# Kernel optimization log

Measured on AMD Instinct MI355X. Metric: run time of the kernel, lower is better.

The kernel has to match this reference:

```python
import jax, jax.numpy as jnp
import numpy as np

N, E = 50000, 800000
IN_CH, HID, OUT, EDIM = 151, 128, 51, 51


def setup_inputs() -> dict:
    key = jax.random.key(0)
    ks = jax.random.split(key, 10)
    def w(k, shape, fan_in):
        return jax.random.normal(k, shape, jnp.float32) * (1.0 / np.sqrt(fan_in))
    return {
        "x": jax.random.normal(ks[0], (N, IN_CH), jnp.float32),
        "edge_attr": jax.random.normal(ks[1], (E, EDIM), jnp.float32),
        "W_edge0": w(ks[2], (EDIM, IN_CH), EDIM),
        "b_edge0": jnp.zeros((IN_CH,), jnp.float32),
        "W0": w(ks[3], (IN_CH, HID), IN_CH),
        "b0": jnp.zeros((HID,), jnp.float32),
        "W_edge1": w(ks[4], (EDIM, HID), EDIM),
        "b_edge1": jnp.zeros((HID,), jnp.float32),
        "W1": w(ks[5], (HID, HID), HID),
        "b1": jnp.zeros((HID,), jnp.float32),
        "W_out": w(ks[6], (HID, OUT), HID),
        "b_out": jnp.zeros((OUT,), jnp.float32),
        "edge_index": jax.random.randint(ks[7], (2, E), 0, N, jnp.int32),
    }


def gtn_layer(x, src, dst, edge_attr, W_e, b_e, W, b):
    # message: x_j + Linear(edge_attr);  aggr='add' scatter to dst.
    eat = edge_attr @ W_e + b_e                                # [E, in_ch]
    msgs = x[src] + eat                                        # gather + add
    agg = jax.ops.segment_sum(msgs, dst, num_segments=x.shape[0])
    # self-loops carry zero edge_attr -> transformed attr == bias b_e,
    # so their message is x + b_e (equivalent to concatenating N self-loop edges).
    agg = agg + x + b_e
    return agg @ W + b                                         # self.linear


def reference(x, edge_attr, W_edge0, b_edge0, W0, b0, W_edge1, b_edge1, W1, b1, W_out, b_out, edge_index):
    src, dst = edge_index[0], edge_index[1]
    h = gtn_layer(x, src, dst, edge_attr, W_edge0, b_edge0, W0, b0)   # [N, HID]
    h = gtn_layer(h, src, dst, edge_attr, W_edge1, b_edge1, W1, b1)   # [N, HID]
    # global_mean_pool with batch=arange(N) is identity (one node per graph)
    return h @ W_out + b_out                                          # [N, OUT]
```

## Files before the change

kernel.cpp:

```cpp
#include <hip/hip_runtime.h>

#define N_NODES 50000
#define N_EDGES 800000
#define IN_CH   151
#define HID     128
#define OUT_CH  51
#define EDIM    51
#define SSTR    52
#define WP      64
#define LSTR    68
#define NBLK    ((N_NODES + 255) / 256)
#define EBLK    ((N_EDGES + 255) / 256)
#define KW1_T   (51 * 128 + 128 + 128 * WP)
#define KW1_B   ((KW1_T + 255) / 256)
#define KW2_T   (51 * WP + 102)
#define KW2_B   ((KW2_T + 255) / 256)

static __device__ __forceinline__ unsigned int f2bf(float f) {
    union { float f; unsigned int u; } v; v.f = f;
    unsigned int r = v.u + 0x7FFF + ((v.u >> 16) & 1);
    return r >> 16;
}
static __device__ __forceinline__ float bflo(unsigned int u) {
    return __uint_as_float(u << 16);
}
static __device__ __forceinline__ float bfhi(unsigned int u) {
    return __uint_as_float(u & 0xFFFF0000u);
}

__global__ void k_hist_kw1(const int* __restrict__ ei, int* __restrict__ deg,
                           const float* __restrict__ We0, const float* __restrict__ W0,
                           const float* __restrict__ be0, const float* __restrict__ W1,
                           const float* __restrict__ Wout,
                           float* __restrict__ M0, float* __restrict__ c0,
                           float* __restrict__ Wc) {
    if (blockIdx.x < EBLK) {
        int e = blockIdx.x * 256 + threadIdx.x;
        if (e < N_EDGES) atomicAdd(&deg[ei[N_EDGES + e]], 1);
        return;
    }
    int t = (blockIdx.x - EBLK) * 256 + threadIdx.x;
    if (t < 51 * 128) {
        int i = t / 128, j = t % 128;
        float a = 0.f;
        for (int k = 0; k < IN_CH; ++k) a += We0[i * IN_CH + k] * W0[k * HID + j];
        M0[t] = a;
    } else if (t < 51 * 128 + 128) {
        int j = t - 51 * 128;
        float a = 0.f;
        for (int k = 0; k < IN_CH; ++k) a += be0[k] * W0[k * HID + j];
        c0[j] = a;
    } else if (t < 51 * 128 + 128 + 128 * WP) {
        int u = t - (51 * 128 + 128);
        int i = u / WP, j = u % WP;
        float a = 0.f;
        if (j < OUT_CH)
            for (int k = 0; k < HID; ++k) a += W1[i * HID + k] * Wout[k * OUT_CH + j];
        Wc[i * WP + j] = a;
    }
}

__global__ void k_scan1_kw2(const int* __restrict__ deg, int* __restrict__ blksum,
                            const float* __restrict__ We1, const float* __restrict__ be1,
                            const float* __restrict__ b1, const float* __restrict__ Wout,
                            const float* __restrict__ bout, const float* __restrict__ Wc,
                            float* __restrict__ Mc, float* __restrict__ cc,
                            float* __restrict__ dd) {
    if (blockIdx.x < NBLK) {
        __shared__ int lds[256];
        int i = blockIdx.x * 256 + threadIdx.x;
        lds[threadIdx.x] = (i < N_NODES) ? deg[i] : 0;
        __syncthreads();
        for (int s = 128; s > 0; s >>= 1) {
            if (threadIdx.x < s) lds[threadIdx.x] += lds[threadIdx.x + s];
            __syncthreads();
        }
        if (threadIdx.x == 0) blksum[blockIdx.x] = lds[0];
        return;
    }
    int t = (blockIdx.x - NBLK) * 256 + threadIdx.x;
    if (t < 51 * WP) {
        int i = t / WP, j = t % WP;
        float a = 0.f;
        if (j < OUT_CH)
            for (int k = 0; k < HID; ++k) a += We1[i * HID + k] * Wc[k * WP + j];
        Mc[t] = a;
    } else if (t < 51 * WP + 51) {
        int j = t - 51 * WP;
        float a = 0.f;
        for (int k = 0; k < HID; ++k) a += be1[k] * Wc[k * WP + j];
        cc[j] = a;
    } else if (t < 51 * WP + 102) {
        int j = t - (51 * WP + 51);
        float a = 0.f;
        for (int k = 0; k < HID; ++k) a += b1[k] * Wout[k * OUT_CH + j];
        dd[j] = a + bout[j];
    }
}

__global__ void k_scan3m(const int* __restrict__ deg, const int* __restrict__ blksum,
                         int* __restrict__ row_start, int* __restrict__ cursor) {
    __shared__ int lds[256];
    __shared__ int s_off;
    int tid = threadIdx.x;
    int v2 = (tid < NBLK) ? blksum[tid] : 0;
    lds[tid] = v2;
    __syncthreads();
    for (int s = 1; s < 256; s <<= 1) {
        int t = (tid >= s) ? lds[tid - s] : 0;
        __syncthreads();
        lds[tid] += t;
        __syncthreads();
    }
    if (tid == 0) s_off = (blockIdx.x == 0) ? 0 : lds[blockIdx.x - 1];
    __syncthreads();
    int boff = s_off;
    int i = blockIdx.x * 256 + tid;
    int v = (i < N_NODES) ? deg[i] : 0;
    lds[tid] = v;
    __syncthreads();
    for (int s = 1; s < 256; s <<= 1) {
        int t = (tid >= s) ? lds[tid - s] : 0;
        __syncthreads();
        lds[tid] += t;
        __syncthreads();
    }
    if (i < N_NODES) {
        int ex = boff + lds[tid] - v;
        row_start[i] = ex;
        cursor[i] = ex;
    }
    if (blockIdx.x == 0 && tid == 0) row_start[N_NODES] = N_EDGES;
}

__global__ void k_fill(const int* __restrict__ ei, int* __restrict__ cursor,
                       int2* __restrict__ pairs) {
    int e = blockIdx.x * 256 + threadIdx.x;
    if (e >= N_EDGES) return;
    int src = ei[e];
    int dst = ei[N_EDGES + e];
    int pos = atomicAdd(&cursor[dst], 1);
    pairs[pos] = make_int2(src, e);
}

__global__ void k_agg_S(const float* __restrict__ ea, const int2* __restrict__ pairs,
                        const int* __restrict__ row_start, float* __restrict__ S) {
    int n = blockIdx.x * 4 + (threadIdx.x >> 6);
    if (n >= N_NODES) return;
    int lane = threadIdx.x & 63;
    int g = lane >> 4, sub = lane & 15;
    int n0 = row_start[n], n1 = row_start[n + 1];
    float4 acc = make_float4(0.f, 0.f, 0.f, 0.f);
    for (int base = n0; base < n1; base += 64) {
        int cnt = min(64, n1 - base);
        int eid_l = (base + lane < n1) ? pairs[base + lane].y : 0;
        for (int t = 0; t < cnt; t += 4) {
            int idx = t + g;
            bool ok = idx < cnt;
            int e = __shfl(eid_l, ok ? idx : 0);
            if (ok && sub < 13) {
                float4 v = *(const float4*)(ea + (size_t)e * EDIM + sub * 4);
                if (sub == 12) v.w = 0.f;
                acc.x += v.x; acc.y += v.y; acc.z += v.z; acc.w += v.w;
            }
        }
    }
    acc.x += __shfl_xor(acc.x, 16); acc.y += __shfl_xor(acc.y, 16);
    acc.z += __shfl_xor(acc.z, 16); acc.w += __shfl_xor(acc.w, 16);
    acc.x += __shfl_xor(acc.x, 32); acc.y += __shfl_xor(acc.y, 32);
    acc.z += __shfl_xor(acc.z, 32); acc.w += __shfl_xor(acc.w, 32);
    if (lane < 13)
        *(float4*)(S + (size_t)n * SSTR + lane * 4) = acc;
}

__global__ void k_agg_h(const uint4* __restrict__ yb4, const int2* __restrict__ pairs,
                        const int* __restrict__ row_start, float* __restrict__ hacc) {
    int n = blockIdx.x * 4 + (threadIdx.x >> 6);
    if (n >= N_NODES) return;
    int lane = threadIdx.x & 63;
    int g = lane >> 4, s = lane & 15;
    int n0 = row_start[n], n1 = row_start[n + 1];
    float acc[8];
#pragma unroll
    for (int j = 0; j < 8; ++j) acc[j] = 0.f;
    for (int base = n0; base < n1; base += 64) {
        int cnt = min(64, n1 - base);
        int s_l = (base + lane < n1) ? pairs[base + lane].x : 0;
        for (int t = 0; t < cnt; t += 4) {
            int idx = t + g;
            bool ok = idx < cnt;
            int srcn = __shfl(s_l, ok ? idx : 0);
            if (ok) {
                uint4 v = yb4[(size_t)srcn * 16 + s];
                acc[0] += bflo(v.x); acc[1] += bfhi(v.x);
                acc[2] += bflo(v.y); acc[3] += bfhi(v.y);
                acc[4] += bflo(v.z); acc[5] += bfhi(v.z);
                acc[6] += bflo(v.w); acc[7] += bfhi(v.w);
            }
        }
    }
#pragma unroll
    for (int j = 0; j < 8; ++j) {
        acc[j] += __shfl_xor(acc[j], 16);
        acc[j] += __shfl_xor(acc[j], 32);
    }
    if (lane < 16) {
        float4* hp = (float4*)(hacc + (size_t)n * HID + lane * 8);
        float4 a = hp[0], b = hp[1];
        a.x += acc[0]; a.y += acc[1]; a.z += acc[2]; a.w += acc[3];
        b.x += acc[4]; b.y += acc[5]; b.z += acc[6]; b.w += acc[7];
        hp[0] = a; hp[1] = b;
    }
}

__global__ void k_agg_out(const uint4* __restrict__ wb4, const int2* __restrict__ pairs,
                          const int* __restrict__ row_start, float* __restrict__ out) {
    int n = blockIdx.x * 4 + (threadIdx.x >> 6);
    if (n >= N_NODES) return;
    int lane = threadIdx.x & 63;
    int g = lane >> 3, s = lane & 7;
    int n0 = row_start[n], n1 = row_start[n + 1];
    float acc[8];
#pragma unroll
    for (int j = 0; j < 8; ++j) acc[j] = 0.f;
    for (int base = n0; base < n1; base += 64) {
        int cnt = min(64, n1 - base);
        int s_l = (base + lane < n1) ? pairs[base + lane].x : 0;
        for (int t = 0; t < cnt; t += 8) {
            int idx = t + g;
            bool ok = idx < cnt;
            int srcn = __shfl(s_l, ok ? idx : 0);
            if (ok) {
                uint4 v = wb4[(size_t)srcn * 8 + s];
                acc[0] += bflo(v.x); acc[1] += bfhi(v.x);
                acc[2] += bflo(v.y); acc[3] += bfhi(v.y);
                acc[4] += bflo(v.z); acc[5] += bfhi(v.z);
                acc[6] += bflo(v.w); acc[7] += bfhi(v.w);
            }
        }
    }
#pragma unroll
    for (int j = 0; j < 8; ++j) {
        acc[j] += __shfl_xor(acc[j], 8);
        acc[j] += __shfl_xor(acc[j], 16);
        acc[j] += __shfl_xor(acc[j], 32);
    }
    if (lane < 8) {
#pragma unroll
        for (int j = 0; j < 8; ++j) {
            int ch = lane * 8 + j;
            if (ch < OUT_CH) out[(size_t)n * OUT_CH + ch] += acc[j];
        }
    }
}

__global__ __launch_bounds__(256, 4) void k_layer0(
        const float* __restrict__ x, const float* __restrict__ W0,
        const float* __restrict__ b0, const float* __restrict__ S,
        const int* __restrict__ deg, const float* __restrict__ M0,
        const float* __restrict__ c0,
        unsigned int* __restrict__ yb, float* __restrict__ hacc) {
    __shared__ float aT[64 * LSTR];
    int tid = threadIdx.x;
    int r_base = blockIdx.x * 64;
    int cg = tid & 15, rg = tid >> 4;
    int c = cg * 8, r0 = rg * 4;

    float4 accA[4], accB[4];
#pragma unroll
    for (int i = 0; i < 4; ++i) {
        accA[i] = make_float4(0.f, 0.f, 0.f, 0.f);
        accB[i] = make_float4(0.f, 0.f, 0.f, 0.f);
    }

    for (int p = 0; p < 3; ++p) {
        int koff = p * 64;
        int chunk = min(64, IN_CH - koff);
        __syncthreads();
        for (int idx = tid; idx < 64 * 64; idx += 256) {
            int r = idx >> 6, kk = idx & 63;
            if (kk >= chunk) continue;
            int row = r_base + r;
            aT[kk * LSTR + r] = (row < N_NODES) ? x[(size_t)row * IN_CH + koff + kk] : 0.f;
        }
        __syncthreads();
#pragma unroll 4
        for (int kk = 0; kk < chunk; ++kk) {
            int k = koff + kk;
            float4 wv0 = *(const float4*)(W0 + k * HID + c);
            float4 wv1 = *(const float4*)(W0 + k * HID + c + 4);
            float4 a0 = *(const float4*)(&aT[kk * LSTR + r0]);
            float ar[4] = {a0.x, a0.y, a0.z, a0.w};
#pragma unroll
            for (int i = 0; i < 4; ++i) {
                accA[i].x += ar[i] * wv0.x; accA[i].y += ar[i] * wv0.y;
                accA[i].z += ar[i] * wv0.z; accA[i].w += ar[i] * wv0.w;
                accB[i].x += ar[i] * wv1.x; accB[i].y += ar[i] * wv1.y;
                accB[i].z += ar[i] * wv1.z; accB[i].w += ar[i] * wv1.w;
            }
        }
    }

#pragma unroll
    for (int i = 0; i < 4; ++i) {
        int row = r_base + r0 + i;
        if (row < N_NODES) {
            uint4 pk;
            pk.x = f2bf(accA[i].x) | (f2bf(accA[i].y) << 16);
            pk.y = f2bf(accA[i].z) | (f2bf(accA[i].w) << 16);
            pk.z = f2bf(accB[i].x) | (f2bf(accB[i].y) << 16);
            pk.w = f2bf(accB[i].z) | (f2bf(accB[i].w) << 16);
            *(uint4*)(yb + (size_t)row * 64 + (c >> 1)) = pk;
        }
    }

    __syncthreads();
    for (int idx = tid; idx < 64 * 64; idx += 256) {
        int r = idx >> 6, kk = idx & 63;
        if (kk >= EDIM) continue;
        int row = r_base + r;
        aT[kk * LSTR + r] = (row < N_NODES) ? S[(size_t)row * SSTR + kk] : 0.f;
    }
    __syncthreads();
#pragma unroll 4
    for (int kk = 0; kk < EDIM; ++kk) {
        float4 wv0 = *(const float4*)(M0 + kk * HID + c);
        float4 wv1 = *(const float4*)(M0 + kk * HID + c + 4);
        float4 a0 = *(const float4*)(&aT[kk * LSTR + r0]);
        float ar[4] = {a0.x, a0.y, a0.z, a0.w};
#pragma unroll
        for (int i = 0; i < 4; ++i) {
            accA[i].x += ar[i] * wv0.x; accA[i].y += ar[i] * wv0.y;
            accA[i].z += ar[i] * wv0.z; accA[i].w += ar[i] * wv0.w;
            accB[i].x += ar[i] * wv1.x; accB[i].y += ar[i] * wv1.y;
            accB[i].z += ar[i] * wv1.z; accB[i].w += ar[i] * wv1.w;
        }
    }

    float4 cv0 = *(const float4*)(c0 + c);
    float4 cv1 = *(const float4*)(c0 + c + 4);
    float4 bv0 = *(const float4*)(b0 + c);
    float4 bv1 = *(const float4*)(b0 + c + 4);
#pragma unroll
    for (int i = 0; i < 4; ++i) {
        int row = r_base + r0 + i;
        if (row < N_NODES) {
            float d1 = (float)(deg[row] + 1);
            float4 vA = accA[i], vB = accB[i];
            vA.x += d1 * cv0.x + bv0.x; vA.y += d1 * cv0.y + bv0.y;
            vA.z += d1 * cv0.z + bv0.z; vA.w += d1 * cv0.w + bv0.w;
            vB.x += d1 * cv1.x + bv1.x; vB.y += d1 * cv1.y + bv1.y;
            vB.z += d1 * cv1.z + bv1.z; vB.w += d1 * cv1.w + bv1.w;
            *(float4*)(hacc + (size_t)row * HID + c) = vA;
            *(float4*)(hacc + (size_t)row * HID + c + 4) = vB;
        }
    }
}

__global__ __launch_bounds__(256, 4) void k_layer1(
        const float* __restrict__ hacc, const float* __restrict__ Wc,
        const float* __restrict__ S, const int* __restrict__ deg,
        const float* __restrict__ Mc, const float* __restrict__ cc,
        const float* __restrict__ dd,
        unsigned int* __restrict__ wb, float* __restrict__ out) {
    __shared__ float aT[64 * LSTR];
    int tid = threadIdx.x;
    int r_base = blockIdx.x * 64;
    int cg = tid & 15, rg = tid >> 4;
    int c = cg * 4, r0 = rg * 4;

    float4 acc[4];
#pragma unroll
    for (int i = 0; i < 4; ++i) acc[i] = make_float4(0.f, 0.f, 0.f, 0.f);

    for (int p = 0; p < 2; ++p) {
        int koff = p * 64;
        __syncthreads();
        for (int idx = tid; idx < 64 * 64; idx += 256) {
            int r = idx >> 6, kk = idx & 63;
            int row = r_base + r;
            aT[kk * LSTR + r] = (row < N_NODES) ? hacc[(size_t)row * HID + koff + kk] : 0.f;
        }
        __syncthreads();
#pragma unroll 4
        for (int kk = 0; kk < 64; ++kk) {
            int k = koff + kk;
            float4 wv = *(const float4*)(Wc + k * WP + c);
            float4 a0 = *(const float4*)(&aT[kk * LSTR + r0]);
            float ar[4] = {a0.x, a0.y, a0.z, a0.w};
#pragma unroll
            for (int i = 0; i < 4; ++i) {
                acc[i].x += ar[i] * wv.x; acc[i].y += ar[i] * wv.y;
                acc[i].z += ar[i] * wv.z; acc[i].w += ar[i] * wv.w;
            }
        }
    }

#pragma unroll
    for (int i = 0; i < 4; ++i) {
        int row = r_base + r0 + i;
        if (row < N_NODES) {
            uint2 pk;
            pk.x = f2bf(acc[i].x) | (f2bf(acc[i].y) << 16);
            pk.y = f2bf(acc[i].z) | (f2bf(acc[i].w) << 16);
            *(uint2*)(wb + (size_t)row * 32 + (c >> 1)) = pk;
        }
    }

    __syncthreads();
    for (int idx = tid; idx < 64 * 64; idx += 256) {
        int r = idx >> 6, kk = idx & 63;
        if (kk >= EDIM) continue;
        int row = r_base + r;
        aT[kk * LSTR + r] = (row < N_NODES) ? S[(size_t)row * SSTR + kk] : 0.f;
    }
    __syncthreads();
#pragma unroll 4
    for (int kk = 0; kk < EDIM; ++kk) {
        float4 wv = *(const float4*)(Mc + kk * WP + c);
        float4 a0 = *(const float4*)(&aT[kk * LSTR + r0]);
        float ar[4] = {a0.x, a0.y, a0.z, a0.w};
#pragma unroll
        for (int i = 0; i < 4; ++i) {
            acc[i].x += ar[i] * wv.x; acc[i].y += ar[i] * wv.y;
            acc[i].z += ar[i] * wv.z; acc[i].w += ar[i] * wv.w;
        }
    }

    if (c < OUT_CH) {
        float cv[4], dv[4];
#pragma unroll
        for (int j = 0; j < 4; ++j) {
            int col = c + j;
            cv[j] = (col < OUT_CH) ? cc[col] : 0.f;
            dv[j] = (col < OUT_CH) ? dd[col] : 0.f;
        }
#pragma unroll
        for (int i = 0; i < 4; ++i) {
            int row = r_base + r0 + i;
            if (row < N_NODES) {
                float d1 = (float)(deg[row] + 1);
                const float* ap = (const float*)&acc[i];
#pragma unroll
                for (int j = 0; j < 4; ++j) {
                    int col = c + j;
                    if (col < OUT_CH)
                        out[(size_t)row * OUT_CH + col] = ap[j] + d1 * cv[j] + dv[j];
                }
            }
        }
    }
}

extern "C" void kernel_launch(void* const* d_in, const int* in_sizes, int n_in,
                              void* d_out, int out_size, void* d_ws, size_t ws_size,
                              hipStream_t stream) {
    const float* x    = (const float*)d_in[0];
    const float* ea   = (const float*)d_in[1];
    const float* We0  = (const float*)d_in[2];
    const float* be0  = (const float*)d_in[3];
    const float* W0   = (const float*)d_in[4];
    const float* b0   = (const float*)d_in[5];
    const float* We1  = (const float*)d_in[6];
    const float* be1  = (const float*)d_in[7];
    const float* W1   = (const float*)d_in[8];
    const float* b1   = (const float*)d_in[9];
    const float* Wout = (const float*)d_in[10];
    const float* bout = (const float*)d_in[11];
    const int*   ei   = (const int*)d_in[12];
    float* out = (float*)d_out;

    char* p = (char*)d_ws;
    auto alloc = [&](size_t bytes) {
        char* r = p;
        p += (bytes + 255) & ~(size_t)255;
        return r;
    };
    float* S         = (float*)alloc((size_t)N_NODES * SSTR * 4);
    int*   deg       = (int*)  alloc((size_t)N_NODES * 4);
    int*   row_start = (int*)  alloc((size_t)(N_NODES + 1) * 4);
    int*   cursor    = (int*)  alloc((size_t)N_NODES * 4);
    int*   blksum    = (int*)  alloc((size_t)NBLK * 4);
    int2*  pairs     = (int2*) alloc((size_t)N_EDGES * 8);
    unsigned int* yb = (unsigned int*)alloc((size_t)N_NODES * 64 * 4);
    float* hacc      = (float*)alloc((size_t)N_NODES * HID * 4);
    unsigned int* wb = (unsigned int*)alloc((size_t)N_NODES * 32 * 4);
    float* M0        = (float*)alloc(51 * 128 * 4);
    float* c0        = (float*)alloc(128 * 4);
    float* Wc        = (float*)alloc(128 * WP * 4);
    float* Mc        = (float*)alloc(51 * WP * 4);
    float* cc        = (float*)alloc(51 * 4);
    float* dd        = (float*)alloc(51 * 4);

    hipMemsetAsync(deg, 0, (size_t)N_NODES * 4, stream);

    k_hist_kw1<<<EBLK + KW1_B, 256, 0, stream>>>(ei, deg, We0, W0, be0, W1, Wout, M0, c0, Wc);
    k_scan1_kw2<<<NBLK + KW2_B, 256, 0, stream>>>(deg, blksum, We1, be1, b1, Wout, bout,
                                                  Wc, Mc, cc, dd);
    k_scan3m<<<NBLK, 256, 0, stream>>>(deg, blksum, row_start, cursor);
    k_fill<<<EBLK, 256, 0, stream>>>(ei, cursor, pairs);

    k_agg_S<<<(N_NODES + 3) / 4, 256, 0, stream>>>(ea, pairs, row_start, S);

    k_layer0<<<(N_NODES + 63) / 64, 256, 0, stream>>>(x, W0, b0, S, deg, M0, c0, yb, hacc);
    k_agg_h<<<(N_NODES + 3) / 4, 256, 0, stream>>>((const uint4*)yb, pairs, row_start, hacc);

    k_layer1<<<(N_NODES + 63) / 64, 256, 0, stream>>>(hacc, Wc, S, deg, Mc, cc, dd, wb, out);
    k_agg_out<<<(N_NODES + 3) / 4, 256, 0, stream>>>((const uint4*)wb, pairs, row_start, out);
}
```

Before: 587.2 us.

## Fuse edge-attr and neighbor aggregation into layer GEMM kernels

Moves the per-node edge_attr sum (S) into the start of the layer-0 GEMM kernel and the bf16 neighbor-feature gather into the start of the layer-1 GEMM kernel. Each block first aggregates its own 64 nodes, then reuses the result. Layer 1 keeps the gathered sums in a 32KB shared tile, which avoids a read-modify-write of hacc in global memory and removes two launches. In exchange, parallelism for the irregular gather drops from 4 nodes per block to 16 nodes per wave, which can hurt latency hiding. The extra shared memory also lowers occupancy, so launch bounds change to 3.

```diff
diff --git a/kernel.cpp b/kernel.cpp
--- a/kernel.cpp
+++ b/kernel.cpp
@@ -143,76 +143,6 @@
     pairs[pos] = make_int2(src, e);
 }
 
-__global__ void k_agg_S(const float* __restrict__ ea, const int2* __restrict__ pairs,
-                        const int* __restrict__ row_start, float* __restrict__ S) {
-    int n = blockIdx.x * 4 + (threadIdx.x >> 6);
-    if (n >= N_NODES) return;
-    int lane = threadIdx.x & 63;
-    int g = lane >> 4, sub = lane & 15;
-    int n0 = row_start[n], n1 = row_start[n + 1];
-    float4 acc = make_float4(0.f, 0.f, 0.f, 0.f);
-    for (int base = n0; base < n1; base += 64) {
-        int cnt = min(64, n1 - base);
-        int eid_l = (base + lane < n1) ? pairs[base + lane].y : 0;
-        for (int t = 0; t < cnt; t += 4) {
-            int idx = t + g;
-            bool ok = idx < cnt;
-            int e = __shfl(eid_l, ok ? idx : 0);
-            if (ok && sub < 13) {
-                float4 v = *(const float4*)(ea + (size_t)e * EDIM + sub * 4);
-                if (sub == 12) v.w = 0.f;
-                acc.x += v.x; acc.y += v.y; acc.z += v.z; acc.w += v.w;
-            }
-        }
-    }
-    acc.x += __shfl_xor(acc.x, 16); acc.y += __shfl_xor(acc.y, 16);
-    acc.z += __shfl_xor(acc.z, 16); acc.w += __shfl_xor(acc.w, 16);
-    acc.x += __shfl_xor(acc.x, 32); acc.y += __shfl_xor(acc.y, 32);
-    acc.z += __shfl_xor(acc.z, 32); acc.w += __shfl_xor(acc.w, 32);
-    if (lane < 13)
-        *(float4*)(S + (size_t)n * SSTR + lane * 4) = acc;
-}
-
-__global__ void k_agg_h(const uint4* __restrict__ yb4, const int2* __restrict__ pairs,
-                        const int* __restrict__ row_start, float* __restrict__ hacc) {
-    int n = blockIdx.x * 4 + (threadIdx.x >> 6);
-    if (n >= N_NODES) return;
-    int lane = threadIdx.x & 63;
-    int g = lane >> 4, s = lane & 15;
-    int n0 = row_start[n], n1 = row_start[n + 1];
-    float acc[8];
-#pragma unroll
-    for (int j = 0; j < 8; ++j) acc[j] = 0.f;
-    for (int base = n0; base < n1; base += 64) {
-        int cnt = min(64, n1 - base);
-        int s_l = (base + lane < n1) ? pairs[base + lane].x : 0;
-        for (int t = 0; t < cnt; t += 4) {
-            int idx = t + g;
-            bool ok = idx < cnt;
-            int srcn = __shfl(s_l, ok ? idx : 0);
-            if (ok) {
-                uint4 v = yb4[(size_t)srcn * 16 + s];
-                acc[0] += bflo(v.x); acc[1] += bfhi(v.x);
-                acc[2] += bflo(v.y); acc[3] += bfhi(v.y);
-                acc[4] += bflo(v.z); acc[5] += bfhi(v.z);
-                acc[6] += bflo(v.w); acc[7] += bfhi(v.w);
-            }
-        }
-    }
-#pragma unroll
-    for (int j = 0; j < 8; ++j) {
-        acc[j] += __shfl_xor(acc[j], 16);
-        acc[j] += __shfl_xor(acc[j], 32);
-    }
-    if (lane < 16) {
-        float4* hp = (float4*)(hacc + (size_t)n * HID + lane * 8);
-        float4 a = hp[0], b = hp[1];
-        a.x += acc[0]; a.y += acc[1]; a.z += acc[2]; a.w += acc[3];
-        b.x += acc[4]; b.y += acc[5]; b.z += acc[6]; b.w += acc[7];
-        hp[0] = a; hp[1] = b;
-    }
-}
-
 __global__ void k_agg_out(const uint4* __restrict__ wb4, const int2* __restrict__ pairs,
                           const int* __restrict__ row_start, float* __restrict__ out) {
     int n = blockIdx.x * 4 + (threadIdx.x >> 6);
@@ -254,15 +184,50 @@
     }
 }
 
-__global__ __launch_bounds__(256, 4) void k_layer0(
+__global__ __launch_bounds__(256, 4) void k_layer0f(
         const float* __restrict__ x, const float* __restrict__ W0,
-        const float* __restrict__ b0, const float* __restrict__ S,
+        const float* __restrict__ b0, const float* __restrict__ ea,
+        const int2* __restrict__ pairs, const int* __restrict__ row_start,
         const int* __restrict__ deg, const float* __restrict__ M0,
-        const float* __restrict__ c0,
+        const float* __restrict__ c0, float* __restrict__ S,
         unsigned int* __restrict__ yb, float* __restrict__ hacc) {
     __shared__ float aT[64 * LSTR];
     int tid = threadIdx.x;
     int r_base = blockIdx.x * 64;
+
+    {
+        int wv = tid >> 6;
+        int lane = tid & 63;
+        int g = lane >> 4, sub = lane & 15;
+        for (int u = 0; u < 16; ++u) {
+            int n = r_base + wv * 16 + u;
+            if (n >= N_NODES) break;
+            int n0 = row_start[n], n1 = row_start[n + 1];
+            float4 acc = make_float4(0.f, 0.f, 0.f, 0.f);
+            for (int base = n0; base < n1; base += 64) {
+                int cnt = min(64, n1 - base);
+                int eid_l = (base + lane < n1) ? pairs[base + lane].y : 0;
+                for (int t = 0; t < cnt; t += 4) {
+                    int idx = t + g;
+                    bool ok = idx < cnt;
+                    int e = __shfl(eid_l, ok ? idx : 0);
+                    if (ok && sub < 13) {
+                        float4 v = *(const float4*)(ea + (size_t)e * EDIM + sub * 4);
+                        if (sub == 12) v.w = 0.f;
+                        acc.x += v.x; acc.y += v.y; acc.z += v.z; acc.w += v.w;
+                    }
+                }
+            }
+            acc.x += __shfl_xor(acc.x, 16); acc.y += __shfl_xor(acc.y, 16);
+            acc.z += __shfl_xor(acc.z, 16); acc.w += __shfl_xor(acc.w, 16);
+            acc.x += __shfl_xor(acc.x, 32); acc.y += __shfl_xor(acc.y, 32);
+            acc.z += __shfl_xor(acc.z, 32); acc.w += __shfl_xor(acc.w, 32);
+            if (lane < 13)
+                *(float4*)(S + (size_t)n * SSTR + lane * 4) = acc;
+        }
+    }
+    __syncthreads();
+
     int cg = tid & 15, rg = tid >> 4;
     int c = cg * 8, r0 = rg * 4;
 
@@ -357,15 +322,59 @@
     }
 }
 
-__global__ __launch_bounds__(256, 4) void k_layer1(
+__global__ __launch_bounds__(256, 3) void k_layer1f(
         const float* __restrict__ hacc, const float* __restrict__ Wc,
         const float* __restrict__ S, const int* __restrict__ deg,
         const float* __restrict__ Mc, const float* __restrict__ cc,
-        const float* __restrict__ dd,
+        const float* __restrict__ dd, const uint4* __restrict__ yb4,
+        const int2* __restrict__ pairs, const int* __restrict__ row_start,
         unsigned int* __restrict__ wb, float* __restrict__ out) {
     __shared__ float aT[64 * LSTR];
+    __shared__ float gt[64 * 128];
     int tid = threadIdx.x;
     int r_base = blockIdx.x * 64;
+
+    {
+        int wv = tid >> 6;
+        int lane = tid & 63;
+        int g = lane >> 4, s = lane & 15;
+        for (int u = 0; u < 16; ++u) {
+            int n = r_base + wv * 16 + u;
+            if (n >= N_NODES) break;
+            int n0 = row_start[n], n1 = row_start[n + 1];
+            float acc[8];
+#pragma unroll
+            for (int j = 0; j < 8; ++j) acc[j] = 0.f;
+            for (int base = n0; base < n1; base += 64) {
+                int cnt = min(64, n1 - base);
+                int s_l = (base + lane < n1) ? pairs[base + lane].x : 0;
+                for (int t = 0; t < cnt; t += 4) {
+                    int idx = t + g;
+                    bool ok = idx < cnt;
+                    int srcn = __shfl(s_l, ok ? idx : 0);
+                    if (ok) {
+                        uint4 v = yb4[(size_t)srcn * 16 + s];
+                        acc[0] += bflo(v.x); acc[1] += bfhi(v.x);
+                        acc[2] += bflo(v.y); acc[3] += bfhi(v.y);
+                        acc[4] += bflo(v.z); acc[5] += bfhi(v.z);
+                        acc[6] += bflo(v.w); acc[7] += bfhi(v.w);
+                    }
+                }
+            }
+#pragma unroll
+            for (int j = 0; j < 8; ++j) {
+                acc[j] += __shfl_xor(acc[j], 16);
+                acc[j] += __shfl_xor(acc[j], 32);
+            }
+            if (lane < 16) {
+                float* gp = gt + (wv * 16 + u) * 128 + lane * 8;
+                *(float4*)(gp)     = make_float4(acc[0], acc[1], acc[2], acc[3]);
+                *(float4*)(gp + 4) = make_float4(acc[4], acc[5], acc[6], acc[7]);
+            }
+        }
+    }
+    __syncthreads();
+
     int cg = tid & 15, rg = tid >> 4;
     int c = cg * 4, r0 = rg * 4;
 
@@ -379,7 +388,9 @@
         for (int idx = tid; idx < 64 * 64; idx += 256) {
             int r = idx >> 6, kk = idx & 63;
             int row = r_base + r;
-            aT[kk * LSTR + r] = (row < N_NODES) ? hacc[(size_t)row * HID + koff + kk] : 0.f;
+            aT[kk * LSTR + r] = (row < N_NODES)
+                ? hacc[(size_t)row * HID + koff + kk] + gt[r * 128 + koff + kk]
+                : 0.f;
         }
         __syncthreads();
 #pragma unroll 4
@@ -500,11 +511,11 @@
     k_scan3m<<<NBLK, 256, 0, stream>>>(deg, blksum, row_start, cursor);
     k_fill<<<EBLK, 256, 0, stream>>>(ei, cursor, pairs);
 
-    k_agg_S<<<(N_NODES + 3) / 4, 256, 0, stream>>>(ea, pairs, row_start, S);
-
-    k_layer0<<<(N_NODES + 63) / 64, 256, 0, stream>>>(x, W0, b0, S, deg, M0, c0, yb, hacc);
-    k_agg_h<<<(N_NODES + 3) / 4, 256, 0, stream>>>((const uint4*)yb, pairs, row_start, hacc);
-
-    k_layer1<<<(N_NODES + 63) / 64, 256, 0, stream>>>(hacc, Wc, S, deg, Mc, cc, dd, wb, out);
+    k_layer0f<<<(N_NODES + 63) / 64, 256, 0, stream>>>(
+        x, W0, b0, ea, pairs, row_start, deg, M0, c0, S, yb, hacc);
+
+    k_layer1f<<<(N_NODES + 63) / 64, 256, 0, stream>>>(
+        hacc, Wc, S, deg, Mc, cc, dd, (const uint4*)yb, pairs, row_start, wb, out);
+
     k_agg_out<<<(N_NODES + 3) / 4, 256, 0, stream>>>((const uint4*)wb, pairs, row_start, out);
 }
```

Measured after the change: 670.6 us. 14.2% more time.

## Replace CSR gather of edge attrs with atomic scatter-add and shrink edge list

Applied to the files above, without the earlier changes.

The per-destination CSR gather of edge_attr rows into S is replaced by a grid-stride kernel that streams edge_attr linearly and atomically adds each element into S at its destination row. The CSR edge list now stores only source ids instead of (src, edge id) pairs, halving that buffer's traffic in fill and the two aggregation kernels. S is zeroed together with deg in one memset. The change trades random 204-byte row gathers for coalesced reads plus about 40M float atomics, which can contend and makes the S sums order-nondeterministic.

```diff
diff --git a/kernel.cpp b/kernel.cpp
--- a/kernel.cpp
+++ b/kernel.cpp
@@ -134,46 +134,29 @@
 }
 
 __global__ void k_fill(const int* __restrict__ ei, int* __restrict__ cursor,
-                       int2* __restrict__ pairs) {
+                       int* __restrict__ srcs) {
     int e = blockIdx.x * 256 + threadIdx.x;
     if (e >= N_EDGES) return;
     int src = ei[e];
     int dst = ei[N_EDGES + e];
     int pos = atomicAdd(&cursor[dst], 1);
-    pairs[pos] = make_int2(src, e);
-}
-
-__global__ void k_agg_S(const float* __restrict__ ea, const int2* __restrict__ pairs,
-                        const int* __restrict__ row_start, float* __restrict__ S) {
-    int n = blockIdx.x * 4 + (threadIdx.x >> 6);
-    if (n >= N_NODES) return;
-    int lane = threadIdx.x & 63;
-    int g = lane >> 4, sub = lane & 15;
-    int n0 = row_start[n], n1 = row_start[n + 1];
-    float4 acc = make_float4(0.f, 0.f, 0.f, 0.f);
-    for (int base = n0; base < n1; base += 64) {
-        int cnt = min(64, n1 - base);
-        int eid_l = (base + lane < n1) ? pairs[base + lane].y : 0;
-        for (int t = 0; t < cnt; t += 4) {
-            int idx = t + g;
-            bool ok = idx < cnt;
-            int e = __shfl(eid_l, ok ? idx : 0);
-            if (ok && sub < 13) {
-                float4 v = *(const float4*)(ea + (size_t)e * EDIM + sub * 4);
-                if (sub == 12) v.w = 0.f;
-                acc.x += v.x; acc.y += v.y; acc.z += v.z; acc.w += v.w;
-            }
-        }
-    }
-    acc.x += __shfl_xor(acc.x, 16); acc.y += __shfl_xor(acc.y, 16);
-    acc.z += __shfl_xor(acc.z, 16); acc.w += __shfl_xor(acc.w, 16);
-    acc.x += __shfl_xor(acc.x, 32); acc.y += __shfl_xor(acc.y, 32);
-    acc.z += __shfl_xor(acc.z, 32); acc.w += __shfl_xor(acc.w, 32);
-    if (lane < 13)
-        *(float4*)(S + (size_t)n * SSTR + lane * 4) = acc;
-}
-
-__global__ void k_agg_h(const uint4* __restrict__ yb4, const int2* __restrict__ pairs,
+    srcs[pos] = src;
+}
+
+__global__ void k_scatter_S(const float* __restrict__ ea, const int* __restrict__ ei,
+                            float* __restrict__ S) {
+    const unsigned int TOT = (unsigned int)N_EDGES * EDIM;
+    unsigned int stride = gridDim.x * blockDim.x;
+    for (unsigned int i = blockIdx.x * blockDim.x + threadIdx.x; i < TOT; i += stride) {
+        unsigned int e = i / EDIM;
+        unsigned int c = i - e * EDIM;
+        float v = ea[i];
+        int dst = ei[N_EDGES + e];
+        atomicAdd(&S[(size_t)dst * SSTR + c], v);
+    }
+}
+
+__global__ void k_agg_h(const uint4* __restrict__ yb4, const int* __restrict__ srcs,
                         const int* __restrict__ row_start, float* __restrict__ hacc) {
     int n = blockIdx.x * 4 + (threadIdx.x >> 6);
     if (n >= N_NODES) return;
@@ -185,7 +168,7 @@
     for (int j = 0; j < 8; ++j) acc[j] = 0.f;
     for (int base = n0; base < n1; base += 64) {
         int cnt = min(64, n1 - base);
-        int s_l = (base + lane < n1) ? pairs[base + lane].x : 0;
+        int s_l = (base + lane < n1) ? srcs[base + lane] : 0;
         for (int t = 0; t < cnt; t += 4) {
             int idx = t + g;
             bool ok = idx < cnt;
@@ -213,7 +196,7 @@
     }
 }
 
-__global__ void k_agg_out(const uint4* __restrict__ wb4, const int2* __restrict__ pairs,
+__global__ void k_agg_out(const uint4* __restrict__ wb4, const int* __restrict__ srcs,
                           const int* __restrict__ row_start, float* __restrict__ out) {
     int n = blockIdx.x * 4 + (threadIdx.x >> 6);
     if (n >= N_NODES) return;
@@ -225,7 +208,7 @@
     for (int j = 0; j < 8; ++j) acc[j] = 0.f;
     for (int base = n0; base < n1; base += 64) {
         int cnt = min(64, n1 - base);
-        int s_l = (base + lane < n1) ? pairs[base + lane].x : 0;
+        int s_l = (base + lane < n1) ? srcs[base + lane] : 0;
         for (int t = 0; t < cnt; t += 8) {
             int idx = t + g;
             bool ok = idx < cnt;
@@ -476,12 +459,13 @@
         p += (bytes + 255) & ~(size_t)255;
         return r;
     };
+    int*   deg       = (int*)  alloc((size_t)N_NODES * 4);
     float* S         = (float*)alloc((size_t)N_NODES * SSTR * 4);
-    int*   deg       = (int*)  alloc((size_t)N_NODES * 4);
+    size_t zspan     = (size_t)((char*)(S + (size_t)N_NODES * SSTR) - (char*)deg);
     int*   row_start = (int*)  alloc((size_t)(N_NODES + 1) * 4);
     int*   cursor    = (int*)  alloc((size_t)N_NODES * 4);
     int*   blksum    = (int*)  alloc((size_t)NBLK * 4);
-    int2*  pairs     = (int2*) alloc((size_t)N_EDGES * 8);
+    int*   srcs      = (int*)  alloc((size_t)N_EDGES * 4);
     unsigned int* yb = (unsigned int*)alloc((size_t)N_NODES * 64 * 4);
     float* hacc      = (float*)alloc((size_t)N_NODES * HID * 4);
     unsigned int* wb = (unsigned int*)alloc((size_t)N_NODES * 32 * 4);
@@ -492,19 +476,19 @@
     float* cc        = (float*)alloc(51 * 4);
     float* dd        = (float*)alloc(51 * 4);
 
-    hipMemsetAsync(deg, 0, (size_t)N_NODES * 4, stream);
+    hipMemsetAsync(deg, 0, zspan, stream);
 
     k_hist_kw1<<<EBLK + KW1_B, 256, 0, stream>>>(ei, deg, We0, W0, be0, W1, Wout, M0, c0, Wc);
     k_scan1_kw2<<<NBLK + KW2_B, 256, 0, stream>>>(deg, blksum, We1, be1, b1, Wout, bout,
                                                   Wc, Mc, cc, dd);
     k_scan3m<<<NBLK, 256, 0, stream>>>(deg, blksum, row_start, cursor);
-    k_fill<<<EBLK, 256, 0, stream>>>(ei, cursor, pairs);
-
-    k_agg_S<<<(N_NODES + 3) / 4, 256, 0, stream>>>(ea, pairs, row_start, S);
+    k_fill<<<EBLK, 256, 0, stream>>>(ei, cursor, srcs);
+
+    k_scatter_S<<<4096, 256, 0, stream>>>(ea, ei, S);
 
     k_layer0<<<(N_NODES + 63) / 64, 256, 0, stream>>>(x, W0, b0, S, deg, M0, c0, yb, hacc);
-    k_agg_h<<<(N_NODES + 3) / 4, 256, 0, stream>>>((const uint4*)yb, pairs, row_start, hacc);
+    k_agg_h<<<(N_NODES + 3) / 4, 256, 0, stream>>>((const uint4*)yb, srcs, row_start, hacc);
 
     k_layer1<<<(N_NODES + 63) / 64, 256, 0, stream>>>(hacc, Wc, S, deg, Mc, cc, dd, wb, out);
-    k_agg_out<<<(N_NODES + 3) / 4, 256, 0, stream>>>((const uint4*)wb, pairs, row_start, out);
-}
+    k_agg_out<<<(N_NODES + 3) / 4, 256, 0, stream>>>((const uint4*)wb, srcs, row_start, out);
+}
```

New measurement: 707.5 us. +20.5%, slower.

## Split bf16 gather tables into 32-channel planes and aggregate per plane

Applied to the files above, without the earlier changes.

Layer outputs are now stored in separate 32-channel planes (64-byte rows) rather than one interleaved row per node. The gather aggregation runs as one kernel launch per plane, with 16 edges in flight per wave. Each launch's table (3.2 MB) is meant to fit better in L2/MALL, raising the cache hit rate of the random gathers. In exchange the edge lists and row offsets are re-read once per plane, more kernels are launched, and the shuffle reductions get longer.

```diff
diff --git a/kernel.cpp b/kernel.cpp
--- a/kernel.cpp
+++ b/kernel.cpp
@@ -9,6 +9,8 @@
 #define SSTR    52
 #define WP      64
 #define LSTR    68
+#define YPQ     ((size_t)N_NODES * 16)
+#define WPQ     ((size_t)N_NODES * 16)
 #define NBLK    ((N_NODES + 255) / 256)
 #define EBLK    ((N_EDGES + 255) / 256)
 #define KW1_T   (51 * 128 + 128 + 128 * WP)
@@ -173,12 +175,13 @@
         *(float4*)(S + (size_t)n * SSTR + lane * 4) = acc;
 }
 
-__global__ void k_agg_h(const uint4* __restrict__ yb4, const int2* __restrict__ pairs,
-                        const int* __restrict__ row_start, float* __restrict__ hacc) {
+__global__ void k_agg_h_p(const uint4* __restrict__ yq, const int2* __restrict__ pairs,
+                          const int* __restrict__ row_start, float* __restrict__ hacc,
+                          int coff) {
     int n = blockIdx.x * 4 + (threadIdx.x >> 6);
     if (n >= N_NODES) return;
     int lane = threadIdx.x & 63;
-    int g = lane >> 4, s = lane & 15;
+    int g = lane >> 2, s = lane & 3;
     int n0 = row_start[n], n1 = row_start[n + 1];
     float acc[8];
 #pragma unroll
@@ -186,12 +189,12 @@
     for (int base = n0; base < n1; base += 64) {
         int cnt = min(64, n1 - base);
         int s_l = (base + lane < n1) ? pairs[base + lane].x : 0;
-        for (int t = 0; t < cnt; t += 4) {
+        for (int t = 0; t < cnt; t += 16) {
             int idx = t + g;
             bool ok = idx < cnt;
             int srcn = __shfl(s_l, ok ? idx : 0);
             if (ok) {
-                uint4 v = yb4[(size_t)srcn * 16 + s];
+                uint4 v = yq[(size_t)srcn * 4 + s];
                 acc[0] += bflo(v.x); acc[1] += bfhi(v.x);
                 acc[2] += bflo(v.y); acc[3] += bfhi(v.y);
                 acc[4] += bflo(v.z); acc[5] += bfhi(v.z);
@@ -201,11 +204,13 @@
     }
 #pragma unroll
     for (int j = 0; j < 8; ++j) {
+        acc[j] += __shfl_xor(acc[j], 4);
+        acc[j] += __shfl_xor(acc[j], 8);
         acc[j] += __shfl_xor(acc[j], 16);
         acc[j] += __shfl_xor(acc[j], 32);
     }
-    if (lane < 16) {
-        float4* hp = (float4*)(hacc + (size_t)n * HID + lane * 8);
+    if (lane < 4) {
+        float4* hp = (float4*)(hacc + (size_t)n * HID + coff + lane * 8);
         float4 a = hp[0], b = hp[1];
         a.x += acc[0]; a.y += acc[1]; a.z += acc[2]; a.w += acc[3];
         b.x += acc[4]; b.y += acc[5]; b.z += acc[6]; b.w += acc[7];
@@ -213,12 +218,13 @@
     }
 }
 
-__global__ void k_agg_out(const uint4* __restrict__ wb4, const int2* __restrict__ pairs,
-                          const int* __restrict__ row_start, float* __restrict__ out) {
+__global__ void k_agg_out_p(const uint4* __restrict__ wq, const int2* __restrict__ pairs,
+                            const int* __restrict__ row_start, float* __restrict__ out,
+                            int coff) {
     int n = blockIdx.x * 4 + (threadIdx.x >> 6);
     if (n >= N_NODES) return;
     int lane = threadIdx.x & 63;
-    int g = lane >> 3, s = lane & 7;
+    int g = lane >> 2, s = lane & 3;
     int n0 = row_start[n], n1 = row_start[n + 1];
     float acc[8];
 #pragma unroll
@@ -226,12 +232,12 @@
     for (int base = n0; base < n1; base += 64) {
         int cnt = min(64, n1 - base);
         int s_l = (base + lane < n1) ? pairs[base + lane].x : 0;
-        for (int t = 0; t < cnt; t += 8) {
+        for (int t = 0; t < cnt; t += 16) {
             int idx = t + g;
             bool ok = idx < cnt;
             int srcn = __shfl(s_l, ok ? idx : 0);
             if (ok) {
-                uint4 v = wb4[(size_t)srcn * 8 + s];
+                uint4 v = wq[(size_t)srcn * 4 + s];
                 acc[0] += bflo(v.x); acc[1] += bfhi(v.x);
                 acc[2] += bflo(v.y); acc[3] += bfhi(v.y);
                 acc[4] += bflo(v.z); acc[5] += bfhi(v.z);
@@ -241,14 +247,15 @@
     }
 #pragma unroll
     for (int j = 0; j < 8; ++j) {
+        acc[j] += __shfl_xor(acc[j], 4);
         acc[j] += __shfl_xor(acc[j], 8);
         acc[j] += __shfl_xor(acc[j], 16);
         acc[j] += __shfl_xor(acc[j], 32);
     }
-    if (lane < 8) {
+    if (lane < 4) {
 #pragma unroll
         for (int j = 0; j < 8; ++j) {
-            int ch = lane * 8 + j;
+            int ch = coff + lane * 8 + j;
             if (ch < OUT_CH) out[(size_t)n * OUT_CH + ch] += acc[j];
         }
     }
@@ -301,16 +308,21 @@
         }
     }
 
-#pragma unroll
-    for (int i = 0; i < 4; ++i) {
-        int row = r_base + r0 + i;
-        if (row < N_NODES) {
-            uint4 pk;
-            pk.x = f2bf(accA[i].x) | (f2bf(accA[i].y) << 16);
-            pk.y = f2bf(accA[i].z) | (f2bf(accA[i].w) << 16);
-            pk.z = f2bf(accB[i].x) | (f2bf(accB[i].y) << 16);
-            pk.w = f2bf(accB[i].z) | (f2bf(accB[i].w) << 16);
-            *(uint4*)(yb + (size_t)row * 64 + (c >> 1)) = pk;
+    {
+        int q = c >> 5;
+        int uoff = (c & 31) >> 1;
+        unsigned int* yp = yb + (size_t)q * YPQ;
+#pragma unroll
+        for (int i = 0; i < 4; ++i) {
+            int row = r_base + r0 + i;
+            if (row < N_NODES) {
+                uint4 pk;
+                pk.x = f2bf(accA[i].x) | (f2bf(accA[i].y) << 16);
+                pk.y = f2bf(accA[i].z) | (f2bf(accA[i].w) << 16);
+                pk.z = f2bf(accB[i].x) | (f2bf(accB[i].y) << 16);
+                pk.w = f2bf(accB[i].z) | (f2bf(accB[i].w) << 16);
+                *(uint4*)(yp + (size_t)row * 16 + uoff) = pk;
+            }
         }
     }
 
@@ -396,14 +408,19 @@
         }
     }
 
-#pragma unroll
-    for (int i = 0; i < 4; ++i) {
-        int row = r_base + r0 + i;
-        if (row < N_NODES) {
-            uint2 pk;
-            pk.x = f2bf(acc[i].x) | (f2bf(acc[i].y) << 16);
-            pk.y = f2bf(acc[i].z) | (f2bf(acc[i].w) << 16);
-            *(uint2*)(wb + (size_t)row * 32 + (c >> 1)) = pk;
+    {
+        int q = c >> 5;
+        int uoff = (c & 31) >> 1;
+        unsigned int* wp = wb + (size_t)q * WPQ;
+#pragma unroll
+        for (int i = 0; i < 4; ++i) {
+            int row = r_base + r0 + i;
+            if (row < N_NODES) {
+                uint2 pk;
+                pk.x = f2bf(acc[i].x) | (f2bf(acc[i].y) << 16);
+                pk.y = f2bf(acc[i].z) | (f2bf(acc[i].w) << 16);
+                *(uint2*)(wp + (size_t)row * 16 + uoff) = pk;
+            }
         }
     }
 
@@ -503,8 +520,14 @@
     k_agg_S<<<(N_NODES + 3) / 4, 256, 0, stream>>>(ea, pairs, row_start, S);
 
     k_layer0<<<(N_NODES + 63) / 64, 256, 0, stream>>>(x, W0, b0, S, deg, M0, c0, yb, hacc);
-    k_agg_h<<<(N_NODES + 3) / 4, 256, 0, stream>>>((const uint4*)yb, pairs, row_start, hacc);
+
+    for (int q = 0; q < 4; ++q)
+        k_agg_h_p<<<(N_NODES + 3) / 4, 256, 0, stream>>>(
+            (const uint4*)(yb + (size_t)q * YPQ), pairs, row_start, hacc, q * 32);
 
     k_layer1<<<(N_NODES + 63) / 64, 256, 0, stream>>>(hacc, Wc, S, deg, Mc, cc, dd, wb, out);
-    k_agg_out<<<(N_NODES + 3) / 4, 256, 0, stream>>>((const uint4*)wb, pairs, row_start, out);
-}
+
+    for (int q = 0; q < 2; ++q)
+        k_agg_out_p<<<(N_NODES + 3) / 4, 256, 0, stream>>>(
+            (const uint4*)(wb + (size_t)q * WPQ), pairs, row_start, out, q * 32);
+}
```

New measurement: 666.9 us. 13.6% more time.
